# Optimization experiments

Measured on AMD Instinct MI355X. Metric: run time of the kernel, lower is better.

## Reference

```python
import jax, jax.numpy as jnp
import numpy as np

N, E, ND, ED, HID, H, L = 50000, 800000, 32, 16, 96, 4, 3
C = HID // H  # per-head channels = 24
NEG_SLOPE = 0.2
LN_EPS = 1e-5


def setup_inputs() -> dict:
    key = jax.random.key(0)
    ks = iter(jax.random.split(key, 40))
    def r(shape, s=0.05):
        return jax.random.normal(next(ks), shape, jnp.float32) * s
    return dict(
        x=r((N, ND), 1.0),
        edge_index=jax.random.randint(next(ks), (2, E), 0, N),
        edge_attr=r((E, ED), 1.0),
        proj_w=r((ND, HID)), proj_b=jnp.zeros((HID,), jnp.float32),
        lin_l_w=r((L, HID, HID)), lin_l_b=jnp.zeros((L, HID), jnp.float32),
        lin_r_w=r((L, HID, HID)), lin_r_b=jnp.zeros((L, HID), jnp.float32),
        lin_e_w=r((L, ED, HID)),
        att=r((L, H, C)),
        conv_b=jnp.zeros((L, HID), jnp.float32),
        ln_g=jnp.ones((L, HID), jnp.float32), ln_b=jnp.zeros((L, HID), jnp.float32),
        head_w1=r((HID, HID // 2)), head_b1=jnp.zeros((HID // 2,), jnp.float32),
        head_w2=r((HID // 2, 1)), head_b2=jnp.zeros((1,), jnp.float32),
    )


def _layernorm(h, g, b):
    mu = h.mean(-1, keepdims=True)
    var = ((h - mu) ** 2).mean(-1, keepdims=True)
    return (h - mu) / jnp.sqrt(var + LN_EPS) * g + b


def _gatv2(x, src, dst, edge_attr, Wl, bl, Wr, br, We, att, bias):
    # GATv2Conv (PyG semantics, eval mode): x_l = lin_l(x) for source, x_r = lin_r(x) for target
    xl = (x @ Wl + bl).reshape(N, H, C)
    xr = (x @ Wr + br).reshape(N, H, C)
    e = (edge_attr @ We).reshape(E, H, C)
    m = jax.nn.leaky_relu(xl[src] + xr[dst] + e, NEG_SLOPE)  # [E,H,C]
    alpha = (m * att).sum(-1)  # [E,H]
    # segment softmax over incoming edges of each target node
    amax = jax.ops.segment_max(alpha, dst, num_segments=N)  # [N,H]
    ea = jnp.exp(alpha - amax[dst])
    denom = jax.ops.segment_sum(ea, dst, num_segments=N)
    alpha = ea / (denom[dst] + 1e-16)
    out = jax.ops.segment_sum(xl[src] * alpha[..., None], dst, num_segments=N)
    return out.reshape(N, HID) + bias


def reference(x, edge_index, edge_attr, proj_w, proj_b, lin_l_w, lin_l_b, lin_r_w,
              lin_r_b, lin_e_w, att, conv_b, ln_g, ln_b, head_w1, head_b1, head_w2, head_b2):
    src, dst = edge_index[0], edge_index[1]
    h = x @ proj_w + proj_b
    for l in range(L):
        m = _gatv2(h, src, dst, edge_attr, lin_l_w[l], lin_l_b[l], lin_r_w[l],
                   lin_r_b[l], lin_e_w[l], att[l], conv_b[l])
        h = _layernorm(h + m, ln_g[l], ln_b[l])
    h = jax.nn.gelu(h @ head_w1 + head_b1, approximate=False)
    return (h @ head_w2 + head_b2).squeeze(-1)
```

## Files before the change

kernel.cpp:

```cpp
#include <hip/hip_runtime.h>

constexpr int N_NODES = 50000;
constexpr int N_EDGES = 800000;
constexpr int ND  = 32;
constexpr int ED  = 16;
constexpr int HID = 96;
constexpr int NLAYER = 3;

typedef unsigned short ushort_t;
typedef unsigned int uint_t;
typedef __attribute__((ext_vector_type(8))) short bf16x8;
typedef __attribute__((ext_vector_type(4))) float f32x4;

__device__ __forceinline__ float bf2f(ushort_t u) {
    union { float f; uint_t ui; } c; c.ui = ((uint_t)u) << 16; return c.f;
}
__device__ __forceinline__ ushort_t f2bf(float f) {
    uint_t u = __float_as_uint(f);
    return (ushort_t)((u + 0x7FFFu + ((u >> 16) & 1u)) >> 16);
}

__global__ void k_count_deg(const int* __restrict__ dst, int* __restrict__ deg) {
    int e4 = blockIdx.x * 256 + threadIdx.x;
    if (e4 * 4 >= N_EDGES) return;
    int4 d = ((const int4*)dst)[e4];
    atomicAdd(&deg[d.x], 1); atomicAdd(&deg[d.y], 1);
    atomicAdd(&deg[d.z], 1); atomicAdd(&deg[d.w], 1);
}

__global__ void k_scan_block(const int* __restrict__ deg, int* __restrict__ rowptr,
                             int* __restrict__ bsum) {
    __shared__ int s[256];
    int i = blockIdx.x * 256 + threadIdx.x;
    int v = (i < N_NODES) ? deg[i] : 0;
    s[threadIdx.x] = v;
    __syncthreads();
    for (int off = 1; off < 256; off <<= 1) {
        int t = (threadIdx.x >= off) ? s[threadIdx.x - off] : 0;
        __syncthreads();
        s[threadIdx.x] += t;
        __syncthreads();
    }
    if (i < N_NODES) rowptr[i] = s[threadIdx.x] - v;
    if (threadIdx.x == 255) bsum[blockIdx.x] = s[255];
}

__global__ void k_scan_bsum(int* __restrict__ bsum, int nb) {
    __shared__ int s[256];
    int t = threadIdx.x;
    int v = (t < nb) ? bsum[t] : 0;
    s[t] = v;
    __syncthreads();
    for (int off = 1; off < 256; off <<= 1) {
        int tv = (t >= off) ? s[t - off] : 0;
        __syncthreads();
        s[t] += tv;
        __syncthreads();
    }
    if (t < nb) bsum[t] = s[t] - v;
}

__global__ void k_scan_add(int* __restrict__ rowptr, const int* __restrict__ bsum) {
    int i = blockIdx.x * 256 + threadIdx.x;
    if (i < N_NODES) rowptr[i] += bsum[blockIdx.x];
    if (i == 0) rowptr[N_NODES] = N_EDGES;
}

__global__ void k_scatter(const int* __restrict__ src, const int* __restrict__ dst,
                          const int* __restrict__ rowptr, int* __restrict__ fill,
                          int* __restrict__ srcs, int* __restrict__ eidxp,
                          int* __restrict__ pdst) {
    int e4 = blockIdx.x * 256 + threadIdx.x;
    if (e4 * 4 >= N_EDGES) return;
    int4 s = ((const int4*)src)[e4];
    int4 d = ((const int4*)dst)[e4];
    int e0 = e4 * 4;
    int p0 = rowptr[d.x] + atomicAdd(&fill[d.x], 1);
    srcs[p0] = s.x; eidxp[p0] = e0;     pdst[p0] = d.x;
    int p1 = rowptr[d.y] + atomicAdd(&fill[d.y], 1);
    srcs[p1] = s.y; eidxp[p1] = e0 + 1; pdst[p1] = d.y;
    int p2 = rowptr[d.z] + atomicAdd(&fill[d.z], 1);
    srcs[p2] = s.z; eidxp[p2] = e0 + 2; pdst[p2] = d.z;
    int p3 = rowptr[d.w] + atomicAdd(&fill[d.w], 1);
    srcs[p3] = s.w; eidxp[p3] = e0 + 3; pdst[p3] = d.w;
}

__global__ void k_perm(const int* __restrict__ eidxp, const float* __restrict__ eattr,
                       ushort_t* __restrict__ ea) {
    int tid = blockIdx.x * 256 + threadIdx.x;
    int p = tid >> 2, q = tid & 3;
    if (p >= N_EDGES) return;
    int e = eidxp[p];
    float4 v = *(const float4*)(eattr + (size_t)e * ED + q * 4);
    uint_t lo = (uint_t)f2bf(v.x) | ((uint_t)f2bf(v.y) << 16);
    uint_t hi = (uint_t)f2bf(v.z) | ((uint_t)f2bf(v.w) << 16);
    *(uint2*)(ea + (size_t)p * ED + q * 4) = make_uint2(lo, hi);
}

__global__ __launch_bounds__(192) void k_proj(const float* __restrict__ x,
                                              const float* __restrict__ pw,
                                              const float* __restrict__ pb,
                                              float* __restrict__ h) {
    int t = threadIdx.x;
    int c = t % 96, half = t / 96;
    float wreg[ND];
#pragma unroll
    for (int k = 0; k < ND; k++) wreg[k] = pw[k * HID + c];
    float b = pb[c];
    int n0 = blockIdx.x * 16 + half * 8;
    for (int i = 0; i < 8; i += 2) {
        int na = n0 + i, nb = na + 1;
        const float4* xa = (const float4*)(x + (size_t)na * ND);
        const float4* xb = (const float4*)(x + (size_t)nb * ND);
        float accA = b, accB = b;
#pragma unroll
        for (int k4 = 0; k4 < ND / 4; k4++) {
            float4 va = xa[k4], vb = xb[k4];
            accA += va.x * wreg[4 * k4] + va.y * wreg[4 * k4 + 1] +
                    va.z * wreg[4 * k4 + 2] + va.w * wreg[4 * k4 + 3];
            accB += vb.x * wreg[4 * k4] + vb.y * wreg[4 * k4 + 1] +
                    vb.z * wreg[4 * k4 + 2] + vb.w * wreg[4 * k4 + 3];
        }
        h[(size_t)na * HID + c] = accA;
        h[(size_t)nb * HID + c] = accB;
    }
}

__global__ __launch_bounds__(256) void k_linlr_mfma(
    const float* __restrict__ h, const float* __restrict__ Wl,
    const float* __restrict__ bl, const float* __restrict__ Wr,
    const float* __restrict__ br, ushort_t* __restrict__ xl,
    ushort_t* __restrict__ xr) {
    __shared__ ushort_t sW[192 * 104];
    __shared__ float sB[192];
    int t = threadIdx.x;

    for (int idx = t; idx < 192 * 96; idx += 256) {
        int n = idx % 192, k = idx / 192;
        float v = (n < 96) ? Wl[k * 96 + n] : Wr[k * 96 + (n - 96)];
        sW[n * 104 + k] = f2bf(v);
    }
    if (t < 192) sB[t] = (t < 96) ? bl[t] : br[t - 96];
    __syncthreads();

    int wv = t >> 6, lane = t & 63;
    int m0 = blockIdx.x * 64 + wv * 16;
    if (m0 >= N_NODES) return;
    int m = lane & 15, quad = lane >> 4;

    bf16x8 afr[3];
    const float* hrow = h + (size_t)(m0 + m) * HID;
#pragma unroll
    for (int s = 0; s < 3; s++) {
        float4 v0 = *(const float4*)(hrow + s * 32 + quad * 8);
        float4 v1 = *(const float4*)(hrow + s * 32 + quad * 8 + 4);
        bf16x8 a;
        a[0] = (short)f2bf(v0.x); a[1] = (short)f2bf(v0.y);
        a[2] = (short)f2bf(v0.z); a[3] = (short)f2bf(v0.w);
        a[4] = (short)f2bf(v1.x); a[5] = (short)f2bf(v1.y);
        a[6] = (short)f2bf(v1.z); a[7] = (short)f2bf(v1.w);
        afr[s] = a;
    }

#pragma unroll
    for (int nt = 0; nt < 12; nt++) {
        int ch = nt * 16 + m;
        f32x4 acc = {0.f, 0.f, 0.f, 0.f};
#pragma unroll
        for (int s = 0; s < 3; s++) {
            bf16x8 bfr = *(const bf16x8*)(sW + (nt * 16 + m) * 104 + s * 32 + quad * 8);
            acc = __builtin_amdgcn_mfma_f32_16x16x32_bf16(afr[s], bfr, acc, 0, 0, 0);
        }
        float bias = sB[ch];
        ushort_t* dst = (ch < 96) ? (xl + (size_t)(m0 + quad * 4) * HID + ch)
                                  : (xr + (size_t)(m0 + quad * 4) * HID + (ch - 96));
#pragma unroll
        for (int r = 0; r < 4; r++)
            dst[(size_t)r * HID] = f2bf(acc[r] + bias);
    }
}

__global__ __launch_bounds__(256) void k_ev(
    const ushort_t* __restrict__ xlb, const ushort_t* __restrict__ xrb,
    const ushort_t* __restrict__ ea, const int* __restrict__ srcs,
    const int* __restrict__ pdst, const float* __restrict__ WeL,
    const float* __restrict__ attL, float4* __restrict__ ev) {
    int wid = blockIdx.x * 4 + (threadIdx.x >> 6);
    int lane = threadIdx.x & 63;
    int col = lane & 15, quad = lane >> 4;

    bf16x8 afr[6];
#pragma unroll
    for (int mc = 0; mc < 6; mc++) {
        bf16x8 a = {0, 0, 0, 0, 0, 0, 0, 0};
        if (quad < 2) {
#pragma unroll
            for (int j = 0; j < 8; j++)
                a[j] = (short)f2bf(WeL[(quad * 8 + j) * HID + mc * 16 + col]);
        }
        afr[mc] = a;
    }
    float attr[6][4];
#pragma unroll
    for (int mc = 0; mc < 6; mc++)
#pragma unroll
        for (int r = 0; r < 4; r++)
            attr[mc][r] = attL[mc * 16 + quad * 4 + r];

#pragma unroll 2
    for (int b = 0; b < 8; b++) {
        int p0 = wid * 128 + b * 16;
        if (p0 >= N_EDGES) continue;
        int p = p0 + col;
        bf16x8 bfr = {0, 0, 0, 0, 0, 0, 0, 0};
        if (quad < 2)
            bfr = *(const bf16x8*)(ea + (size_t)p * ED + quad * 8);
        f32x4 zero4 = {0.f, 0.f, 0.f, 0.f};
        f32x4 d[6];
#pragma unroll
        for (int mc = 0; mc < 6; mc++)
            d[mc] = __builtin_amdgcn_mfma_f32_16x16x32_bf16(afr[mc], bfr, zero4, 0, 0, 0);

        int src = srcs[p], dst = pdst[p];
        float s[6];
#pragma unroll
        for (int mc = 0; mc < 6; mc++) {
            int cb = mc * 16 + quad * 4;
            uint2 xu = *(const uint2*)(xlb + (size_t)src * HID + cb);
            uint2 ru = *(const uint2*)(xrb + (size_t)dst * HID + cb);
            float x0 = bf2f((ushort_t)(xu.x & 0xffff)), x1 = bf2f((ushort_t)(xu.x >> 16));
            float x2 = bf2f((ushort_t)(xu.y & 0xffff)), x3 = bf2f((ushort_t)(xu.y >> 16));
            float r0 = bf2f((ushort_t)(ru.x & 0xffff)), r1 = bf2f((ushort_t)(ru.x >> 16));
            float r2 = bf2f((ushort_t)(ru.y & 0xffff)), r3 = bf2f((ushort_t)(ru.y >> 16));
            float z0 = x0 + r0 + d[mc][0]; z0 = z0 > 0.f ? z0 : 0.2f * z0;
            float z1 = x1 + r1 + d[mc][1]; z1 = z1 > 0.f ? z1 : 0.2f * z1;
            float z2 = x2 + r2 + d[mc][2]; z2 = z2 > 0.f ? z2 : 0.2f * z2;
            float z3 = x3 + r3 + d[mc][3]; z3 = z3 > 0.f ? z3 : 0.2f * z3;
            s[mc] = z0 * attr[mc][0] + z1 * attr[mc][1] +
                    z2 * attr[mc][2] + z3 * attr[mc][3];
        }
        float U[6], V[6];
#pragma unroll
        for (int mc = 0; mc < 6; mc++) {
            U[mc] = s[mc] + __shfl_xor(s[mc], 16);
            V[mc] = U[mc] + __shfl_xor(U[mc], 32);
        }
        if (quad == 0) {
            float h0 = V[0] + U[1];
            float h1 = (V[1] - U[1]) + V[2];
            float h2 = V[3] + U[4];
            float h3 = (V[4] - U[4]) + V[5];
            ev[p] = make_float4(__expf(h0), __expf(h1), __expf(h2), __expf(h3));
        }
    }
}

__global__ __launch_bounds__(256) void k_agg(
    const ushort_t* __restrict__ xlb, const float* __restrict__ evf,
    const int* __restrict__ srcs, const int* __restrict__ rowptr,
    const float* __restrict__ convb, const float* __restrict__ lng,
    const float* __restrict__ lnb, float* __restrict__ h) {
    int lane = threadIdx.x & 63;
    int node = blockIdx.x * 4 + (threadIdx.x >> 6);
    int slot = lane >> 4, q = lane & 15;
    int c0 = q * 6, head = q >> 2;
    int beg = rowptr[node], end = rowptr[node + 1];
    int cnt = (end - beg + 3) >> 2;

    float n0 = 0.f, n1 = 0.f, n2 = 0.f, n3 = 0.f, n4 = 0.f, n5 = 0.f, den = 0.f;
    if (cnt > 0) {
        int p = beg + slot;
        bool v = p < end;
        int pc = v ? p : beg;
        int src = srcs[pc];
        float evv = evf[4 * pc + head];
        const ushort_t* xp = xlb + (size_t)src * HID + c0;
        uint_t a0 = *(const uint_t*)(xp);
        uint_t a1 = *(const uint_t*)(xp + 2);
        uint_t a2 = *(const uint_t*)(xp + 4);
        for (int it = 0; it < cnt; ++it) {
            int pn = beg + (it + 1) * 4 + slot;
            bool vn = pn < end;
            int pcn = vn ? pn : beg;
            int srcn = srcs[pcn];
            float evn = evf[4 * pcn + head];
            const ushort_t* xpn = xlb + (size_t)srcn * HID + c0;
            uint_t b0 = *(const uint_t*)(xpn);
            uint_t b1 = *(const uint_t*)(xpn + 2);
            uint_t b2 = *(const uint_t*)(xpn + 4);

            float e = v ? evv : 0.f;
            n0 += e * bf2f((ushort_t)(a0 & 0xffff));
            n1 += e * bf2f((ushort_t)(a0 >> 16));
            n2 += e * bf2f((ushort_t)(a1 & 0xffff));
            n3 += e * bf2f((ushort_t)(a1 >> 16));
            n4 += e * bf2f((ushort_t)(a2 & 0xffff));
            n5 += e * bf2f((ushort_t)(a2 >> 16));
            den += e;

            v = vn; evv = evn; a0 = b0; a1 = b1; a2 = b2;
        }
    }
    n0 += __shfl_xor(n0, 16); n0 += __shfl_xor(n0, 32);
    n1 += __shfl_xor(n1, 16); n1 += __shfl_xor(n1, 32);
    n2 += __shfl_xor(n2, 16); n2 += __shfl_xor(n2, 32);
    n3 += __shfl_xor(n3, 16); n3 += __shfl_xor(n3, 32);
    n4 += __shfl_xor(n4, 16); n4 += __shfl_xor(n4, 32);
    n5 += __shfl_xor(n5, 16); n5 += __shfl_xor(n5, 32);
    den += __shfl_xor(den, 16); den += __shfl_xor(den, 32);

    size_t nb = (size_t)node * HID + c0;
    float inv = 1.f / (den + 1e-16f);
    float v0 = h[nb + 0] + n0 * inv + convb[c0 + 0];
    float v1 = h[nb + 1] + n1 * inv + convb[c0 + 1];
    float v2 = h[nb + 2] + n2 * inv + convb[c0 + 2];
    float v3 = h[nb + 3] + n3 * inv + convb[c0 + 3];
    float v4 = h[nb + 4] + n4 * inv + convb[c0 + 4];
    float v5 = h[nb + 5] + n5 * inv + convb[c0 + 5];
    float sm = v0 + v1 + v2 + v3 + v4 + v5;
    sm += __shfl_xor(sm, 1); sm += __shfl_xor(sm, 2);
    sm += __shfl_xor(sm, 4); sm += __shfl_xor(sm, 8);
    float mu = sm * (1.f / 96.f);
    float d0 = v0 - mu, d1 = v1 - mu, d2 = v2 - mu;
    float d3 = v3 - mu, d4 = v4 - mu, d5 = v5 - mu;
    float sv = d0 * d0 + d1 * d1 + d2 * d2 + d3 * d3 + d4 * d4 + d5 * d5;
    sv += __shfl_xor(sv, 1); sv += __shfl_xor(sv, 2);
    sv += __shfl_xor(sv, 4); sv += __shfl_xor(sv, 8);
    float rstd = rsqrtf(sv * (1.f / 96.f) + 1e-5f);
    if (slot == 0) {
        h[nb + 0] = d0 * rstd * lng[c0 + 0] + lnb[c0 + 0];
        h[nb + 1] = d1 * rstd * lng[c0 + 1] + lnb[c0 + 1];
        h[nb + 2] = d2 * rstd * lng[c0 + 2] + lnb[c0 + 2];
        h[nb + 3] = d3 * rstd * lng[c0 + 3] + lnb[c0 + 3];
        h[nb + 4] = d4 * rstd * lng[c0 + 4] + lnb[c0 + 4];
        h[nb + 5] = d5 * rstd * lng[c0 + 5] + lnb[c0 + 5];
    }
}

__global__ __launch_bounds__(256) void k_head_mfma(
    const float* __restrict__ h, const float* __restrict__ W1,
    const float* __restrict__ b1, const float* __restrict__ W2,
    const float* __restrict__ b2, float* __restrict__ out) {
    __shared__ ushort_t sW[48 * 104];
    __shared__ float sB1[48];
    __shared__ float sW2[48];
    int t = threadIdx.x;
    for (int idx = t; idx < 48 * 96; idx += 256) {
        int j = idx % 48, k = idx / 48;
        sW[j * 104 + k] = f2bf(W1[k * 48 + j]);
    }
    if (t < 48) { sB1[t] = b1[t]; sW2[t] = W2[t]; }
    __syncthreads();

    int wv = t >> 6, lane = t & 63;
    int m0 = blockIdx.x * 64 + wv * 16;
    if (m0 >= N_NODES) return;
    int col = lane & 15, quad = lane >> 4;

    bf16x8 afr[3];
    const float* hrow = h + (size_t)(m0 + col) * HID;
#pragma unroll
    for (int s = 0; s < 3; s++) {
        float4 v0 = *(const float4*)(hrow + s * 32 + quad * 8);
        float4 v1 = *(const float4*)(hrow + s * 32 + quad * 8 + 4);
        bf16x8 a;
        a[0] = (short)f2bf(v0.x); a[1] = (short)f2bf(v0.y);
        a[2] = (short)f2bf(v0.z); a[3] = (short)f2bf(v0.w);
        a[4] = (short)f2bf(v1.x); a[5] = (short)f2bf(v1.y);
        a[6] = (short)f2bf(v1.z); a[7] = (short)f2bf(v1.w);
        afr[s] = a;
    }

    const float inv_sqrt2 = 0.70710678118654752f;
    float y0 = 0.f, y1 = 0.f, y2 = 0.f, y3 = 0.f;
#pragma unroll
    for (int nt = 0; nt < 3; nt++) {
        f32x4 acc = {0.f, 0.f, 0.f, 0.f};
#pragma unroll
        for (int s = 0; s < 3; s++) {
            bf16x8 bfr = *(const bf16x8*)(sW + (nt * 16 + col) * 104 + s * 32 + quad * 8);
            acc = __builtin_amdgcn_mfma_f32_16x16x32_bf16(afr[s], bfr, acc, 0, 0, 0);
        }
        int ch = nt * 16 + col;
        float bias = sB1[ch], w2 = sW2[ch];
        float v, g;
        v = acc[0] + bias; g = 0.5f * v * (1.f + erff(v * inv_sqrt2)); y0 += g * w2;
        v = acc[1] + bias; g = 0.5f * v * (1.f + erff(v * inv_sqrt2)); y1 += g * w2;
        v = acc[2] + bias; g = 0.5f * v * (1.f + erff(v * inv_sqrt2)); y2 += g * w2;
        v = acc[3] + bias; g = 0.5f * v * (1.f + erff(v * inv_sqrt2)); y3 += g * w2;
    }
    y0 += __shfl_xor(y0, 1); y0 += __shfl_xor(y0, 2);
    y0 += __shfl_xor(y0, 4); y0 += __shfl_xor(y0, 8);
    y1 += __shfl_xor(y1, 1); y1 += __shfl_xor(y1, 2);
    y1 += __shfl_xor(y1, 4); y1 += __shfl_xor(y1, 8);
    y2 += __shfl_xor(y2, 1); y2 += __shfl_xor(y2, 2);
    y2 += __shfl_xor(y2, 4); y2 += __shfl_xor(y2, 8);
    y3 += __shfl_xor(y3, 1); y3 += __shfl_xor(y3, 2);
    y3 += __shfl_xor(y3, 4); y3 += __shfl_xor(y3, 8);
    if (col == 0) {
        float bb = b2[0];
        out[m0 + quad * 4 + 0] = y0 + bb;
        out[m0 + quad * 4 + 1] = y1 + bb;
        out[m0 + quad * 4 + 2] = y2 + bb;
        out[m0 + quad * 4 + 3] = y3 + bb;
    }
}

extern "C" void kernel_launch(void* const* d_in, const int* in_sizes, int n_in,
                              void* d_out, int out_size, void* d_ws, size_t ws_size,
                              hipStream_t stream) {
    const float* x       = (const float*)d_in[0];
    const int*   eidx    = (const int*)  d_in[1];
    const float* eattr   = (const float*)d_in[2];
    const float* proj_w  = (const float*)d_in[3];
    const float* proj_b  = (const float*)d_in[4];
    const float* lin_l_w = (const float*)d_in[5];
    const float* lin_l_b = (const float*)d_in[6];
    const float* lin_r_w = (const float*)d_in[7];
    const float* lin_r_b = (const float*)d_in[8];
    const float* lin_e_w = (const float*)d_in[9];
    const float* att     = (const float*)d_in[10];
    const float* conv_b  = (const float*)d_in[11];
    const float* ln_g    = (const float*)d_in[12];
    const float* ln_b    = (const float*)d_in[13];
    const float* head_w1 = (const float*)d_in[14];
    const float* head_b1 = (const float*)d_in[15];
    const float* head_w2 = (const float*)d_in[16];
    const float* head_b2 = (const float*)d_in[17];
    float* out = (float*)d_out;

    char* p = (char*)d_ws;
    auto alloc = [&](size_t bytes) -> char* {
        char* r = p;
        p += (bytes + 255) & ~size_t(255);
        return r;
    };
    float*    h      = (float*)alloc(sizeof(float) * (size_t)N_NODES * HID);
    ushort_t* xl     = (ushort_t*)alloc(2 * (size_t)N_NODES * HID);
    ushort_t* xr     = (ushort_t*)alloc(2 * (size_t)N_NODES * HID);
    int*      deg    = (int*)alloc(4 * (size_t)N_NODES);
    int*      fill   = (int*)alloc(4 * (size_t)N_NODES);
    int*      rowptr = (int*)alloc(4 * (size_t)(N_NODES + 1));
    int*      bsum   = (int*)alloc(4 * 256);
    int*      srcs   = (int*)alloc(4 * (size_t)N_EDGES);
    int*      eidxp  = (int*)alloc(4 * (size_t)N_EDGES);
    int*      pdst   = (int*)alloc(4 * (size_t)N_EDGES);
    ushort_t* ea_csr = (ushort_t*)alloc(2 * (size_t)N_EDGES * ED);
    float4*   ev     = (float4*)alloc(16 * (size_t)N_EDGES);

    const int* srcA = eidx;
    const int* dstA = eidx + N_EDGES;

    int ebl4 = (N_EDGES / 4 + 255) / 256;
    int nbl  = (N_NODES + 255) / 256;

    hipMemsetAsync(deg, 0, 4 * (size_t)N_NODES, stream);
    hipMemsetAsync(fill, 0, 4 * (size_t)N_NODES, stream);
    k_count_deg<<<ebl4, 256, 0, stream>>>(dstA, deg);
    k_scan_block<<<nbl, 256, 0, stream>>>(deg, rowptr, bsum);
    k_scan_bsum<<<1, 256, 0, stream>>>(bsum, nbl);
    k_scan_add<<<nbl, 256, 0, stream>>>(rowptr, bsum);
    k_scatter<<<ebl4, 256, 0, stream>>>(srcA, dstA, rowptr, fill, srcs, eidxp, pdst);
    k_perm<<<(N_EDGES * 4) / 256, 256, 0, stream>>>(eidxp, eattr, ea_csr);

    k_proj<<<N_NODES / 16, 192, 0, stream>>>(x, proj_w, proj_b, h);
    for (int l = 0; l < NLAYER; l++) {
        k_linlr_mfma<<<(N_NODES + 63) / 64, 256, 0, stream>>>(
            h, lin_l_w + (size_t)l * HID * HID, lin_l_b + (size_t)l * HID,
            lin_r_w + (size_t)l * HID * HID, lin_r_b + (size_t)l * HID, xl, xr);
        k_ev<<<1563, 256, 0, stream>>>(xl, xr, ea_csr, srcs, pdst,
                                       lin_e_w + (size_t)l * ED * HID,
                                       att + (size_t)l * HID,
                                       (float4*)ev);
        k_agg<<<N_NODES / 4, 256, 0, stream>>>(
            xl, (const float*)ev, srcs, rowptr, conv_b + (size_t)l * HID,
            ln_g + (size_t)l * HID, ln_b + (size_t)l * HID, h);
    }
    k_head_mfma<<<(N_NODES + 63) / 64, 256, 0, stream>>>(h, head_w1, head_b1,
                                                         head_w2, head_b2, out);
}
```

Before: 608.4 us.

## Fuse edge-attr permute into scatter and software-pipeline gathers in k_ev

The scatter kernel now converts each edge's attributes to bf16 and writes them straight to the CSR slot, so the separate permutation kernel and the eidxp array go away. The fill counters are seeded with rowptr inside scan_add, which removes one memset and one rowptr read per edge. In k_ev, each wave loads its src and dst indices once and hands them out with shuffles, and the xl/xr gathers for the next 16-edge batch are double-buffered in registers so they overlap the MFMA and math of the current batch. This raises register pressure, and scatter now does scattered 32-byte writes with less parallelism per thread.

```diff
diff --git a/kernel.cpp b/kernel.cpp
--- a/kernel.cpp
+++ b/kernel.cpp
@@ -60,41 +60,43 @@
     if (t < nb) bsum[t] = s[t] - v;
 }
 
-__global__ void k_scan_add(int* __restrict__ rowptr, const int* __restrict__ bsum) {
+__global__ void k_scan_add(int* __restrict__ rowptr, const int* __restrict__ bsum,
+                           int* __restrict__ fill) {
     int i = blockIdx.x * 256 + threadIdx.x;
-    if (i < N_NODES) rowptr[i] += bsum[blockIdx.x];
+    if (i < N_NODES) {
+        int v = rowptr[i] + bsum[blockIdx.x];
+        rowptr[i] = v;
+        fill[i] = v;
+    }
     if (i == 0) rowptr[N_NODES] = N_EDGES;
 }
 
 __global__ void k_scatter(const int* __restrict__ src, const int* __restrict__ dst,
-                          const int* __restrict__ rowptr, int* __restrict__ fill,
-                          int* __restrict__ srcs, int* __restrict__ eidxp,
-                          int* __restrict__ pdst) {
+                          const float* __restrict__ eattr, int* __restrict__ fill,
+                          int* __restrict__ srcs, int* __restrict__ pdst,
+                          ushort_t* __restrict__ ea) {
     int e4 = blockIdx.x * 256 + threadIdx.x;
     if (e4 * 4 >= N_EDGES) return;
     int4 s = ((const int4*)src)[e4];
     int4 d = ((const int4*)dst)[e4];
     int e0 = e4 * 4;
-    int p0 = rowptr[d.x] + atomicAdd(&fill[d.x], 1);
-    srcs[p0] = s.x; eidxp[p0] = e0;     pdst[p0] = d.x;
-    int p1 = rowptr[d.y] + atomicAdd(&fill[d.y], 1);
-    srcs[p1] = s.y; eidxp[p1] = e0 + 1; pdst[p1] = d.y;
-    int p2 = rowptr[d.z] + atomicAdd(&fill[d.z], 1);
-    srcs[p2] = s.z; eidxp[p2] = e0 + 2; pdst[p2] = d.z;
-    int p3 = rowptr[d.w] + atomicAdd(&fill[d.w], 1);
-    srcs[p3] = s.w; eidxp[p3] = e0 + 3; pdst[p3] = d.w;
-}
-
-__global__ void k_perm(const int* __restrict__ eidxp, const float* __restrict__ eattr,
-                       ushort_t* __restrict__ ea) {
-    int tid = blockIdx.x * 256 + threadIdx.x;
-    int p = tid >> 2, q = tid & 3;
-    if (p >= N_EDGES) return;
-    int e = eidxp[p];
-    float4 v = *(const float4*)(eattr + (size_t)e * ED + q * 4);
-    uint_t lo = (uint_t)f2bf(v.x) | ((uint_t)f2bf(v.y) << 16);
-    uint_t hi = (uint_t)f2bf(v.z) | ((uint_t)f2bf(v.w) << 16);
-    *(uint2*)(ea + (size_t)p * ED + q * 4) = make_uint2(lo, hi);
+    int sv[4] = {s.x, s.y, s.z, s.w};
+    int dv[4] = {d.x, d.y, d.z, d.w};
+#pragma unroll
+    for (int j = 0; j < 4; j++) {
+        int pos = atomicAdd(&fill[dv[j]], 1);
+        srcs[pos] = sv[j];
+        pdst[pos] = dv[j];
+        const float4* er = (const float4*)(eattr + (size_t)(e0 + j) * ED);
+        uint2* ew = (uint2*)(ea + (size_t)pos * ED);
+#pragma unroll
+        for (int q = 0; q < 4; q++) {
+            float4 v = er[q];
+            uint_t lo = (uint_t)f2bf(v.x) | ((uint_t)f2bf(v.y) << 16);
+            uint_t hi = (uint_t)f2bf(v.z) | ((uint_t)f2bf(v.w) << 16);
+            ew[q] = make_uint2(lo, hi);
+        }
+    }
 }
 
 __global__ __launch_bounds__(192) void k_proj(const float* __restrict__ x,
@@ -187,7 +189,12 @@
     const float* __restrict__ attL, float4* __restrict__ ev) {
     int wid = blockIdx.x * 4 + (threadIdx.x >> 6);
     int lane = threadIdx.x & 63;
+    if (wid >= N_EDGES / 128) return;
     int col = lane & 15, quad = lane >> 4;
+    int comp = col & 1, base = col >> 1;
+
+    int2 sp = *(const int2*)(srcs + wid * 128 + 2 * lane);
+    int2 dp = *(const int2*)(pdst + wid * 128 + 2 * lane);
 
     bf16x8 afr[6];
 #pragma unroll
@@ -207,31 +214,51 @@
         for (int r = 0; r < 4; r++)
             attr[mc][r] = attL[mc * 16 + quad * 4 + r];
 
-#pragma unroll 2
+    bf16x8 bfr[2];
+    uint2 xu[2][6], ru[2][6];
+
+    auto getsd = [&](int b, int& sv, int& dv) {
+        int sl = b * 8 + base;
+        int sx = __shfl(sp.x, sl), sy = __shfl(sp.y, sl);
+        int dx = __shfl(dp.x, sl), dy = __shfl(dp.y, sl);
+        sv = comp ? sy : sx;
+        dv = comp ? dy : dx;
+    };
+    auto issue = [&](int b, int pp) {
+        int sv, dv;
+        getsd(b, sv, dv);
+        int p = wid * 128 + b * 16 + col;
+        bf16x8 z8 = {0, 0, 0, 0, 0, 0, 0, 0};
+        bfr[pp] = (quad < 2) ? *(const bf16x8*)(ea + (size_t)p * ED + quad * 8) : z8;
+        const ushort_t* xp = xlb + (size_t)sv * HID + quad * 4;
+        const ushort_t* rp = xrb + (size_t)dv * HID + quad * 4;
+#pragma unroll
+        for (int mc = 0; mc < 6; mc++) {
+            xu[pp][mc] = *(const uint2*)(xp + mc * 16);
+            ru[pp][mc] = *(const uint2*)(rp + mc * 16);
+        }
+    };
+
+    issue(0, 0);
+#pragma unroll
     for (int b = 0; b < 8; b++) {
-        int p0 = wid * 128 + b * 16;
-        if (p0 >= N_EDGES) continue;
-        int p = p0 + col;
-        bf16x8 bfr = {0, 0, 0, 0, 0, 0, 0, 0};
-        if (quad < 2)
-            bfr = *(const bf16x8*)(ea + (size_t)p * ED + quad * 8);
+        int pp = b & 1;
+        if (b < 7) issue(b + 1, pp ^ 1);
+
         f32x4 zero4 = {0.f, 0.f, 0.f, 0.f};
         f32x4 d[6];
 #pragma unroll
         for (int mc = 0; mc < 6; mc++)
-            d[mc] = __builtin_amdgcn_mfma_f32_16x16x32_bf16(afr[mc], bfr, zero4, 0, 0, 0);
-
-        int src = srcs[p], dst = pdst[p];
+            d[mc] = __builtin_amdgcn_mfma_f32_16x16x32_bf16(afr[mc], bfr[pp], zero4, 0, 0, 0);
+
         float s[6];
 #pragma unroll
         for (int mc = 0; mc < 6; mc++) {
-            int cb = mc * 16 + quad * 4;
-            uint2 xu = *(const uint2*)(xlb + (size_t)src * HID + cb);
-            uint2 ru = *(const uint2*)(xrb + (size_t)dst * HID + cb);
-            float x0 = bf2f((ushort_t)(xu.x & 0xffff)), x1 = bf2f((ushort_t)(xu.x >> 16));
-            float x2 = bf2f((ushort_t)(xu.y & 0xffff)), x3 = bf2f((ushort_t)(xu.y >> 16));
-            float r0 = bf2f((ushort_t)(ru.x & 0xffff)), r1 = bf2f((ushort_t)(ru.x >> 16));
-            float r2 = bf2f((ushort_t)(ru.y & 0xffff)), r3 = bf2f((ushort_t)(ru.y >> 16));
+            uint2 a = xu[pp][mc], r = ru[pp][mc];
+            float x0 = bf2f((ushort_t)(a.x & 0xffff)), x1 = bf2f((ushort_t)(a.x >> 16));
+            float x2 = bf2f((ushort_t)(a.y & 0xffff)), x3 = bf2f((ushort_t)(a.y >> 16));
+            float r0 = bf2f((ushort_t)(r.x & 0xffff)), r1 = bf2f((ushort_t)(r.x >> 16));
+            float r2 = bf2f((ushort_t)(r.y & 0xffff)), r3 = bf2f((ushort_t)(r.y >> 16));
             float z0 = x0 + r0 + d[mc][0]; z0 = z0 > 0.f ? z0 : 0.2f * z0;
             float z1 = x1 + r1 + d[mc][1]; z1 = z1 > 0.f ? z1 : 0.2f * z1;
             float z2 = x2 + r2 + d[mc][2]; z2 = z2 > 0.f ? z2 : 0.2f * z2;
@@ -250,6 +277,7 @@
             float h1 = (V[1] - U[1]) + V[2];
             float h2 = V[3] + U[4];
             float h3 = (V[4] - U[4]) + V[5];
+            int p = wid * 128 + b * 16 + col;
             ev[p] = make_float4(__expf(h0), __expf(h1), __expf(h2), __expf(h3));
         }
     }
@@ -442,9 +470,8 @@
     int*      fill   = (int*)alloc(4 * (size_t)N_NODES);
     int*      rowptr = (int*)alloc(4 * (size_t)(N_NODES + 1));
     int*      bsum   = (int*)alloc(4 * 256);
-    int*      srcs   = (int*)alloc(4 * (size_t)N_EDGES);
-    int*      eidxp  = (int*)alloc(4 * (size_t)N_EDGES);
-    int*      pdst   = (int*)alloc(4 * (size_t)N_EDGES);
+    int*      srcs   = (int*)alloc(4 * ((size_t)N_EDGES + 256));
+    int*      pdst   = (int*)alloc(4 * ((size_t)N_EDGES + 256));
     ushort_t* ea_csr = (ushort_t*)alloc(2 * (size_t)N_EDGES * ED);
     float4*   ev     = (float4*)alloc(16 * (size_t)N_EDGES);
 
@@ -455,13 +482,11 @@
     int nbl  = (N_NODES + 255) / 256;
 
     hipMemsetAsync(deg, 0, 4 * (size_t)N_NODES, stream);
-    hipMemsetAsync(fill, 0, 4 * (size_t)N_NODES, stream);
     k_count_deg<<<ebl4, 256, 0, stream>>>(dstA, deg);
     k_scan_block<<<nbl, 256, 0, stream>>>(deg, rowptr, bsum);
     k_scan_bsum<<<1, 256, 0, stream>>>(bsum, nbl);
-    k_scan_add<<<nbl, 256, 0, stream>>>(rowptr, bsum);
-    k_scatter<<<ebl4, 256, 0, stream>>>(srcA, dstA, rowptr, fill, srcs, eidxp, pdst);
-    k_perm<<<(N_EDGES * 4) / 256, 256, 0, stream>>>(eidxp, eattr, ea_csr);
+    k_scan_add<<<nbl, 256, 0, stream>>>(rowptr, bsum, fill);
+    k_scatter<<<ebl4, 256, 0, stream>>>(srcA, dstA, eattr, fill, srcs, pdst, ea_csr);
 
     k_proj<<<N_NODES / 16, 192, 0, stream>>>(x, proj_w, proj_b, h);
     for (int l = 0; l < NLAYER; l++) {
```

Measured after the change: 587.2 us. -3.5%, faster.
